# Optimization experiments

Hardware: AMD Instinct MI355X
Metric: run time of the kernel (lower is better)

Reference implementation:

```python
import jax, jax.numpy as jnp
import numpy as np

B, S, Y = 2, 4, 4          # samples, n_views (B*S = BS), voxel height vox_xyz_size[1]
BS = B * S

def _bilinear(feat, coords):
    # feat: [C,H,W]; coords: [N,2] normalized (x,y); OOB handled by the valid mask
    C, H, W = feat.shape
    gx, gy = coords[:, 0], coords[:, 1]
    ix = (gx + 1.0) * 0.5 * (W - 1)
    iy = (gy + 1.0) * 0.5 * (H - 1)
    x0 = jnp.floor(ix); y0 = jnp.floor(iy)
    wx = ix - x0; wy = iy - y0
    x0i = jnp.clip(x0.astype(jnp.int32), 0, W - 1); x1i = jnp.clip(x0i + 1, 0, W - 1)
    y0i = jnp.clip(y0.astype(jnp.int32), 0, H - 1); y1i = jnp.clip(y0i + 1, 0, H - 1)
    v00 = feat[:, y0i, x0i]; v01 = feat[:, y0i, x1i]
    v10 = feat[:, y1i, x0i]; v11 = feat[:, y1i, x1i]
    out = (v00 * (1 - wx) * (1 - wy) + v01 * wx * (1 - wy)
           + v10 * (1 - wx) * wy + v11 * wx * wy)            # [C,N]
    valid = (gx >= -1) & (gx <= 1) & (gy >= -1) & (gy <= 1)   # [N]
    return out, valid

def _scale(feat, coords, Zs, Xs, w, b):
    # feat: [BS,C,H,W]; coords: [BS, Y*Zs*Xs, 2]; w: [Co, C*Y]; b: [Co]
    C = feat.shape[1]
    samp, valid = jax.vmap(_bilinear)(feat, coords)           # [BS,C,N], [BS,N]
    samp = samp.reshape(BS, C, Y, Zs * Xs)
    masked = samp * valid.reshape(BS, 1, Y, Zs * Xs).astype(samp.dtype)
    v = masked.reshape(B, S, C * Y, Zs * Xs).max(axis=1)      # max-pool across views
    v = v.reshape(B, C * Y, Zs, Xs)                           # BEV grid
    bev = jax.nn.silu(jnp.einsum('bizx,oi->bozx', v, w) + b[None, :, None, None])
    return bev, valid

def setup_inputs():
    key = jax.random.key(0)
    ks = jax.random.split(key, 9)
    f = jnp.float32
    x3 = jax.random.normal(ks[0], (BS, 256, 64, 64), f)
    x4 = jax.random.normal(ks[1], (BS, 512, 32, 32), f)
    x5 = jax.random.normal(ks[2], (BS, 1024, 16, 16), f)
    coords_s2 = jax.random.uniform(ks[3], (BS, Y * 64 * 64, 2), f) * 2.4 - 1.2
    coords_s4 = jax.random.uniform(ks[4], (BS, Y * 32 * 32, 2), f) * 2.4 - 1.2
    coords_s8 = jax.random.uniform(ks[5], (BS, Y * 16 * 16, 2), f) * 2.4 - 1.2
    w2 = jax.random.normal(ks[6], (256, 256 * Y), f) * 0.02
    b2 = jnp.zeros((256,), f)
    w4 = jax.random.normal(ks[7], (512, 512 * Y), f) * 0.02
    b4 = jnp.zeros((512,), f)
    w8 = jax.random.normal(ks[8], (1024, 1024 * Y), f) * 0.02
    b8 = jnp.zeros((1024,), f)
    return {"x3": x3, "x4": x4, "x5": x5,
            "coords_s2": coords_s2, "coords_s4": coords_s4, "coords_s8": coords_s8,
            "w2": w2, "b2": b2, "w4": w4, "b4": b4, "w8": w8, "b8": b8}

def reference(x3, x4, x5, coords_s2, coords_s4, coords_s8, w2, b2, w4, b4, w8, b8):
    bev2, valid2 = _scale(x3, coords_s2, 64, 64, w2, b2)
    bev4, _ = _scale(x4, coords_s4, 32, 32, w4, b4)
    bev8, _ = _scale(x5, coords_s8, 16, 16, w8, b8)
    valid_vox_mask = valid2.reshape(B, S, -1).max(axis=1).astype(jnp.float32)
    return bev2, bev4, bev8, valid_vox_mask
```

## Files before the change

kernel.cpp:

```cpp
#include <hip/hip_runtime.h>
#include <hip/hip_bf16.h>
#include <math.h>

namespace {

typedef short short8 __attribute__((ext_vector_type(8)));
typedef float floatx4 __attribute__((ext_vector_type(4)));
typedef unsigned short ushort4v __attribute__((ext_vector_type(4)));
typedef unsigned short ushort8v __attribute__((ext_vector_type(8)));

__device__ __forceinline__ unsigned short f2bf(float x) {
    union { float f; unsigned u; } a; a.f = x;
    unsigned r = a.u + 0x7fff + ((a.u >> 16) & 1);
    return (unsigned short)(r >> 16);
}
__device__ __forceinline__ float bf2f(unsigned short h) {
    union { unsigned u; float f; } a; a.u = ((unsigned)h) << 16;
    return a.f;
}
__device__ __forceinline__ unsigned f2h(float x) {
    _Float16 h = (_Float16)x;
    unsigned short u; __builtin_memcpy(&u, &h, 2);
    return u;
}
__device__ __forceinline__ float h2f(unsigned u) {
    unsigned short us = (unsigned short)u;
    _Float16 h; __builtin_memcpy(&h, &us, 2);
    return (float)h;
}

__device__ __forceinline__ void transp_tile(
    const float* __restrict__ in, unsigned short* __restrict__ out,
    int C, int P, int bs, int pBase, int cBase, int tid, float (*tile)[33])
{
    int tx = tid & 31;
    int ty = tid >> 5;
    const float* ip = in + ((size_t)bs * C + cBase) * P + pBase;
    #pragma unroll
    for (int r = 0; r < 32; r += 8)
        tile[ty + r][tx] = ip[(size_t)(ty + r) * P + tx];
    __syncthreads();
    unsigned short* op = out + ((size_t)bs * P + pBase) * C + cBase;
    #pragma unroll
    for (int r = 0; r < 32; r += 8)
        op[(size_t)(ty + r) * C + tx] = f2bf(tile[tx][ty + r]);
}

__device__ __forceinline__ void coord_prep(
    const float* __restrict__ coords, uint4* __restrict__ table, int Wd, int idx)
{
    float2 g = ((const float2*)coords)[idx];
    uint4 e;
    bool valid = (g.x >= -1.f) && (g.x <= 1.f) && (g.y >= -1.f) && (g.y <= 1.f);
    if (!valid) {
        e.x = 0xFFFFFFFFu; e.y = 0u; e.z = 0u; e.w = 0u;
    } else {
        float ix = (g.x + 1.f) * 0.5f * (float)(Wd - 1);
        float iy = (g.y + 1.f) * 0.5f * (float)(Wd - 1);
        float x0f = floorf(ix), y0f = floorf(iy);
        float wx = ix - x0f, wy = iy - y0f;
        int x0 = min(max((int)x0f, 0), Wd - 1);
        int x1 = min(x0 + 1, Wd - 1);
        int y0 = min(max((int)y0f, 0), Wd - 1);
        int y1 = min(y0 + 1, Wd - 1);
        unsigned p00 = y0 * Wd + x0, p01 = y0 * Wd + x1;
        unsigned p10 = y1 * Wd + x0, p11 = y1 * Wd + x1;
        e.x = p00 | (p01 << 16);
        e.y = p10 | (p11 << 16);
        e.z = f2h((1.f - wx) * (1.f - wy)) | (f2h(wx * (1.f - wy)) << 16);
        e.w = f2h((1.f - wx) * wy)         | (f2h(wx * wy) << 16);
    }
    table[idx] = e;
}

__global__ __launch_bounds__(256) void prep_all(
    const float* __restrict__ x3, const float* __restrict__ x4, const float* __restrict__ x5,
    unsigned short* __restrict__ f2, unsigned short* __restrict__ f4, unsigned short* __restrict__ f8,
    const float* __restrict__ w2, const float* __restrict__ w4, const float* __restrict__ w8,
    unsigned short* __restrict__ o2, unsigned short* __restrict__ o4, unsigned short* __restrict__ o8,
    const float* __restrict__ c2, const float* __restrict__ c4, const float* __restrict__ c8,
    uint4* __restrict__ t2, uint4* __restrict__ t4, uint4* __restrict__ t8,
    float* __restrict__ mask)
{
    __shared__ float tile[32][33];
    int bid = blockIdx.x;
    int tid = threadIdx.x;
    if (bid < 8192) {
        int bs = bid >> 10, r = bid & 1023;
        transp_tile(x3, f2, 256, 4096, bs, (r & 127) * 32, (r >> 7) * 32, tid, tile);
    } else if (bid < 12288) {
        int local = bid - 8192;
        int bs = local >> 9, r = local & 511;
        transp_tile(x4, f4, 512, 1024, bs, (r & 31) * 32, (r >> 5) * 32, tid, tile);
    } else if (bid < 14336) {
        int local = bid - 12288;
        int bs = local >> 8, r = local & 255;
        transp_tile(x5, f8, 1024, 256, bs, (r & 7) * 32, (r >> 3) * 32, tid, tile);
    } else if (bid < 19712) {
        int local = bid - 14336;
        const float* in; unsigned short* out;
        if (local < 256)       { in = w2; out = o2; }
        else if (local < 1280) { in = w4; out = o4; local -= 256; }
        else                   { in = w8; out = o8; local -= 1280; }
        long idx = ((long)local * 256 + tid) * 4;
        float4 v = *reinterpret_cast<const float4*>(in + idx);
        ushort4 u;
        u.x = f2bf(v.x); u.y = f2bf(v.y); u.z = f2bf(v.z); u.w = f2bf(v.w);
        *reinterpret_cast<ushort4*>(out + idx) = u;
    } else if (bid < 20224) {
        coord_prep(c2, t2, 64, (bid - 19712) * 256 + tid);
    } else if (bid < 20352) {
        coord_prep(c4, t4, 32, (bid - 20224) * 256 + tid);
    } else if (bid < 20384) {
        coord_prep(c8, t8, 16, (bid - 20352) * 256 + tid);
    } else {
        int idx = (bid - 20384) * 256 + tid;
        int n = idx & 16383;
        int b = idx >> 14;
        float best = 0.f;
        #pragma unroll
        for (int s = 0; s < 4; ++s) {
            float2 g = ((const float2*)c2)[(size_t)(b * 4 + s) * 16384 + n];
            bool valid = (g.x >= -1.f) && (g.x <= 1.f) && (g.y >= -1.f) && (g.y <= 1.f);
            if (valid) best = 1.f;
        }
        mask[idx] = best;
    }
}

__device__ __forceinline__ void sample_core(
    const unsigned short* __restrict__ featT, const uint4* __restrict__ table,
    unsigned short* __restrict__ vout,
    int P, int M, int C, int logM, int b, int m, int chunk, int lane)
{
    int c = chunk * 256 + lane * 4;
    unsigned short outv[16];
    #pragma unroll
    for (int y = 0; y < 4; ++y) {
        float bst0 = -3.4e38f, bst1 = -3.4e38f, bst2 = -3.4e38f, bst3 = -3.4e38f;
        bool anyinv = false;
        #pragma unroll
        for (int s = 0; s < 4; ++s) {
            int bs = b * 4 + s;
            uint4 e = table[(((size_t)bs * 4 + y) << logM) + m];
            if ((e.x & 0xffffu) == 0xffffu) { anyinv = true; continue; }
            unsigned p00 = e.x & 0xffffu, p01 = e.x >> 16;
            unsigned p10 = e.y & 0xffffu, p11 = e.y >> 16;
            float w00 = h2f(e.z & 0xffffu), w01 = h2f(e.z >> 16);
            float w10 = h2f(e.w & 0xffffu), w11 = h2f(e.w >> 16);
            const unsigned short* fp = featT + (size_t)bs * P * C + c;
            ushort4v u00 = *reinterpret_cast<const ushort4v*>(fp + (size_t)p00 * C);
            ushort4v u01 = *reinterpret_cast<const ushort4v*>(fp + (size_t)p01 * C);
            ushort4v u10 = *reinterpret_cast<const ushort4v*>(fp + (size_t)p10 * C);
            ushort4v u11 = *reinterpret_cast<const ushort4v*>(fp + (size_t)p11 * C);
            bst0 = fmaxf(bst0, bf2f(u00[0]) * w00 + bf2f(u01[0]) * w01 + bf2f(u10[0]) * w10 + bf2f(u11[0]) * w11);
            bst1 = fmaxf(bst1, bf2f(u00[1]) * w00 + bf2f(u01[1]) * w01 + bf2f(u10[1]) * w10 + bf2f(u11[1]) * w11);
            bst2 = fmaxf(bst2, bf2f(u00[2]) * w00 + bf2f(u01[2]) * w01 + bf2f(u10[2]) * w10 + bf2f(u11[2]) * w11);
            bst3 = fmaxf(bst3, bf2f(u00[3]) * w00 + bf2f(u01[3]) * w01 + bf2f(u10[3]) * w10 + bf2f(u11[3]) * w11);
        }
        if (anyinv) {
            bst0 = fmaxf(bst0, 0.f); bst1 = fmaxf(bst1, 0.f);
            bst2 = fmaxf(bst2, 0.f); bst3 = fmaxf(bst3, 0.f);
        }
        outv[0 * 4 + y] = f2bf(bst0);
        outv[1 * 4 + y] = f2bf(bst1);
        outv[2 * 4 + y] = f2bf(bst2);
        outv[3 * 4 + y] = f2bf(bst3);
    }
    size_t base = (((size_t)b << logM) + m) * ((size_t)C * 4) + (size_t)chunk * 1024 + lane * 16;
    ushort8v o0, o1;
    #pragma unroll
    for (int t = 0; t < 8; ++t) { o0[t] = outv[t]; o1[t] = outv[8 + t]; }
    *reinterpret_cast<ushort8v*>(vout + base)     = o0;
    *reinterpret_cast<ushort8v*>(vout + base + 8) = o1;
}

__global__ __launch_bounds__(256) void sample_all(
    const unsigned short* __restrict__ f2, const unsigned short* __restrict__ f4,
    const unsigned short* __restrict__ f8,
    const uint4* __restrict__ t2, const uint4* __restrict__ t4, const uint4* __restrict__ t8,
    unsigned short* __restrict__ v2, unsigned short* __restrict__ v4,
    unsigned short* __restrict__ v8)
{
    int bid = blockIdx.x;
    int w = threadIdx.x >> 6;
    int lane = threadIdx.x & 63;
    if (bid < 2048) {
        sample_core(f2, t2, v2, 4096, 4096, 256, 12,
                    bid & 1, (bid >> 1) * 4 + w, 0, lane);
    } else if (bid < 3072) {
        int local = bid - 2048;
        sample_core(f4, t4, v4, 1024, 1024, 512, 10,
                    local & 1, (local >> 1) * 2 + (w >> 1), w & 1, lane);
    } else {
        int local = bid - 3072;
        sample_core(f8, t8, v8, 256, 256, 1024, 8,
                    local & 1, local >> 1, w, lane);
    }
}

#define GLOAD(s, it) do { \
    w##s##a = *reinterpret_cast<const float4*>(Wp + (size_t)row0 * K + (it) * 64 + kc); \
    w##s##b = *reinterpret_cast<const float4*>(Wp + (size_t)(row0 + 32) * K + (it) * 64 + kc); \
    v##s##a = *reinterpret_cast<const float4*>(Vp + (size_t)row0 * K + (it) * 64 + kc); \
    v##s##b = *reinterpret_cast<const float4*>(Vp + (size_t)(row0 + 32) * K + (it) * 64 + kc); \
} while (0)

#define LSTORE(s, buf) do { \
    *reinterpret_cast<float4*>(&As[buf][row0 * 72 + kc]) = w##s##a; \
    *reinterpret_cast<float4*>(&As[buf][(row0 + 32) * 72 + kc]) = w##s##b; \
    *reinterpret_cast<float4*>(&Bs[buf][row0 * 72 + kc]) = v##s##a; \
    *reinterpret_cast<float4*>(&Bs[buf][(row0 + 32) * 72 + kc]) = v##s##b; \
} while (0)

#define MFMA_STEP(buf) do { \
    _Pragma("unroll") \
    for (int kss = 0; kss < 64; kss += 32) { \
        short8 af0 = *reinterpret_cast<const short8*>(&As[buf][(wo + lr) * 72 + kss + quad * 8]); \
        short8 af1 = *reinterpret_cast<const short8*>(&As[buf][(wo + 16 + lr) * 72 + kss + quad * 8]); \
        short8 bf0 = *reinterpret_cast<const short8*>(&Bs[buf][(wm + lr) * 72 + kss + quad * 8]); \
        short8 bf1 = *reinterpret_cast<const short8*>(&Bs[buf][(wm + 16 + lr) * 72 + kss + quad * 8]); \
        acc[0][0] = __builtin_amdgcn_mfma_f32_16x16x32_bf16(af0, bf0, acc[0][0], 0, 0, 0); \
        acc[0][1] = __builtin_amdgcn_mfma_f32_16x16x32_bf16(af0, bf1, acc[0][1], 0, 0, 0); \
        acc[1][0] = __builtin_amdgcn_mfma_f32_16x16x32_bf16(af1, bf0, acc[1][0], 0, 0, 0); \
        acc[1][1] = __builtin_amdgcn_mfma_f32_16x16x32_bf16(af1, bf1, acc[1][1], 0, 0, 0); \
    } \
} while (0)

__device__ __forceinline__ void gemm_tile(
    const unsigned short* __restrict__ Wb, const unsigned short* __restrict__ Vb,
    const float* __restrict__ bias, float* __restrict__ out, float* __restrict__ partial,
    int N, int K, int M, int kSplit, int local, int logMt, int logNt,
    int tid, unsigned short (*As)[64 * 72], unsigned short (*Bs)[64 * 72])
{
    const int mTile = local & ((1 << logMt) - 1);
    const int rest  = local >> logMt;
    const int oTile = rest & ((1 << logNt) - 1);
    const int z     = rest >> logNt;
    const int b = z & 1;
    const int ks = z >> 1;
    const int Kspan = K / kSplit;
    const int nIter = Kspan >> 6;

    const int mBase = mTile * 64;
    const int oBase = oTile * 64;
    const int lane = tid & 63;
    const int wave = tid >> 6;
    const int wo = (wave >> 1) * 32;
    const int wm = (wave & 1) * 32;
    const int quad = lane >> 4;
    const int lr = lane & 15;
    const int row0 = tid >> 3;
    const int kc = (tid & 7) * 8;

    const unsigned short* Wp = Wb + (size_t)oBase * K + ks * Kspan;
    const unsigned short* Vp = Vb + ((size_t)b * M + mBase) * K + ks * Kspan;

    floatx4 acc[2][2] = {};
    float4 w0a, w0b, v0a, v0b;
    float4 w1a, w1b, v1a, v1b;

    GLOAD(0, 0);
    LSTORE(0, 0);
    GLOAD(1, 1);
    __syncthreads();

    for (int it = 0; it < nIter; it += 2) {
        MFMA_STEP(0);
        LSTORE(1, 1);
        if (it + 2 < nIter) GLOAD(0, it + 2);
        __syncthreads();
        MFMA_STEP(1);
        if (it + 2 < nIter) {
            LSTORE(0, 0);
            if (it + 3 < nIter) GLOAD(1, it + 3);
            __syncthreads();
        }
    }

    if (kSplit == 1) {
        #pragma unroll
        for (int i = 0; i < 2; ++i)
            #pragma unroll
            for (int r = 0; r < 4; ++r) {
                int o = oBase + wo + i * 16 + quad * 4 + r;
                float bi = bias[o];
                #pragma unroll
                for (int j = 0; j < 2; ++j) {
                    int m = mBase + wm + j * 16 + lr;
                    float x = acc[i][j][r] + bi;
                    out[((size_t)b * N + o) * M + m] = x / (1.f + __expf(-x));
                }
            }
    } else {
        float* pp = partial + (size_t)z * N * M;
        #pragma unroll
        for (int i = 0; i < 2; ++i)
            #pragma unroll
            for (int r = 0; r < 4; ++r) {
                int o = oBase + wo + i * 16 + quad * 4 + r;
                #pragma unroll
                for (int j = 0; j < 2; ++j) {
                    int m = mBase + wm + j * 16 + lr;
                    pp[(size_t)o * M + m] = acc[i][j][r];
                }
            }
    }
}

__global__ __launch_bounds__(256) void gemm_all(
    const unsigned short* __restrict__ w2b, const unsigned short* __restrict__ w4b,
    const unsigned short* __restrict__ w8b,
    const unsigned short* __restrict__ v2, const unsigned short* __restrict__ v4,
    const unsigned short* __restrict__ v8,
    const float* __restrict__ b2, float* __restrict__ bev2,
    float* __restrict__ part4, float* __restrict__ part8)
{
    __shared__ __align__(16) unsigned short As[2][64 * 72];
    __shared__ __align__(16) unsigned short Bs[2][64 * 72];
    int bid = blockIdx.x;
    int tid = threadIdx.x;
    if (bid < 512)
        gemm_tile(w2b, v2, b2, bev2, nullptr, 256, 1024, 4096, 1, bid, 6, 2, tid, As, Bs);
    else if (bid < 1536)
        gemm_tile(w4b, v4, nullptr, nullptr, part4, 512, 2048, 1024, 4, bid - 512, 4, 3, tid, As, Bs);
    else
        gemm_tile(w8b, v8, nullptr, nullptr, part8, 1024, 4096, 256, 8, bid - 1536, 2, 4, tid, As, Bs);
}

__device__ __forceinline__ void reduce_seg(
    const float* __restrict__ partial, const float* __restrict__ bias,
    float* __restrict__ out, int N, int M, int kSplit, size_t idx)
{
    int m4 = M >> 2;
    int mi = (int)(idx % m4);
    int o  = (int)((idx / m4) % N);
    int b  = (int)(idx / ((size_t)m4 * N));
    size_t base = ((size_t)b * N + o) * M + (size_t)mi * 4;
    size_t stride = (size_t)2 * N * M;
    float4 s = *reinterpret_cast<const float4*>(partial + base);
    for (int k = 1; k < kSplit; ++k) {
        float4 t = *reinterpret_cast<const float4*>(partial + base + (size_t)k * stride);
        s.x += t.x; s.y += t.y; s.z += t.z; s.w += t.w;
    }
    float bi = bias[o];
    float xs[4] = {s.x + bi, s.y + bi, s.z + bi, s.w + bi};
    float4 r;
    r.x = xs[0] / (1.f + __expf(-xs[0]));
    r.y = xs[1] / (1.f + __expf(-xs[1]));
    r.z = xs[2] / (1.f + __expf(-xs[2]));
    r.w = xs[3] / (1.f + __expf(-xs[3]));
    *reinterpret_cast<float4*>(out + base) = r;
}

__global__ __launch_bounds__(256) void reduce_all(
    const float* __restrict__ part4, const float* __restrict__ b4, float* __restrict__ bev4,
    const float* __restrict__ part8, const float* __restrict__ b8, float* __restrict__ bev8)
{
    int bid = blockIdx.x;
    int tid = threadIdx.x;
    if (bid < 1024)
        reduce_seg(part4, b4, bev4, 512, 1024, 4, (size_t)bid * 256 + tid);
    else
        reduce_seg(part8, b8, bev8, 1024, 256, 8, (size_t)(bid - 1024) * 256 + tid);
}

}

extern "C" void kernel_launch(void* const* d_in, const int* in_sizes, int n_in,
                              void* d_out, int out_size, void* d_ws, size_t ws_size,
                              hipStream_t stream)
{
    const float* x3 = (const float*)d_in[0];
    const float* x4 = (const float*)d_in[1];
    const float* x5 = (const float*)d_in[2];
    const float* c2 = (const float*)d_in[3];
    const float* c4 = (const float*)d_in[4];
    const float* c8 = (const float*)d_in[5];
    const float* w2 = (const float*)d_in[6];
    const float* b2 = (const float*)d_in[7];
    const float* w4 = (const float*)d_in[8];
    const float* b4 = (const float*)d_in[9];
    const float* w8 = (const float*)d_in[10];
    const float* b8 = (const float*)d_in[11];

    float* out  = (float*)d_out;
    float* bev2 = out;
    float* bev4 = bev2 + (long)2 * 256 * 64 * 64;
    float* bev8 = bev4 + (long)2 * 512 * 32 * 32;
    float* mask = bev8 + (long)2 * 1024 * 16 * 16;

    char* ws = (char*)d_ws;
    unsigned short* f2v  = (unsigned short*)(ws);
    unsigned short* f4v  = (unsigned short*)(ws + (16L << 20));
    unsigned short* f8v  = (unsigned short*)(ws + (24L << 20));
    unsigned short* v2v  = (unsigned short*)(ws + (28L << 20));
    unsigned short* v4v  = (unsigned short*)(ws + (44L << 20));
    unsigned short* v8v  = (unsigned short*)(ws + (52L << 20));
    unsigned short* w2bf = (unsigned short*)(ws + (56L << 20));
    unsigned short* w4bf = (unsigned short*)(ws + (57L << 20));
    unsigned short* w8bf = (unsigned short*)(ws + (59L << 20));
    float*          part4 = (float*)(ws + (68L << 20));
    float*          part8 = (float*)(ws + (84L << 20));
    uint4*          t2v   = (uint4*)(ws + (100L << 20));
    uint4*          t4v   = (uint4*)(ws + (102L << 20));
    uint4*          t8v   = (uint4*)(ws + (102L << 20) + (1L << 19));

    prep_all<<<dim3(20512), 256, 0, stream>>>(
        x3, x4, x5, f2v, f4v, f8v,
        w2, w4, w8, w2bf, w4bf, w8bf,
        c2, c4, c8, t2v, t4v, t8v, mask);
    sample_all<<<dim3(3584), 256, 0, stream>>>(
        f2v, f4v, f8v, t2v, t4v, t8v, v2v, v4v, v8v);
    gemm_all<<<dim3(2560), 256, 0, stream>>>(
        w2bf, w4bf, w8bf, v2v, v4v, v8v, b2, bev2, part4, part8);
    reduce_all<<<dim3(1536), 256, 0, stream>>>(
        part4, b4, bev4, part8, b8, bev8);
}
```

Before: 204.2 us.

## Stagger per-scale stages across kernels to overlap prep, sampling and GEMM

Result: slower. 210.0 us (+2.8%).

```diff
diff --git a/kernel.cpp b/kernel.cpp
--- a/kernel.cpp
+++ b/kernel.cpp
@@ -73,59 +73,14 @@
     table[idx] = e;
 }
 
-__global__ __launch_bounds__(256) void prep_all(
-    const float* __restrict__ x3, const float* __restrict__ x4, const float* __restrict__ x5,
-    unsigned short* __restrict__ f2, unsigned short* __restrict__ f4, unsigned short* __restrict__ f8,
-    const float* __restrict__ w2, const float* __restrict__ w4, const float* __restrict__ w8,
-    unsigned short* __restrict__ o2, unsigned short* __restrict__ o4, unsigned short* __restrict__ o8,
-    const float* __restrict__ c2, const float* __restrict__ c4, const float* __restrict__ c8,
-    uint4* __restrict__ t2, uint4* __restrict__ t4, uint4* __restrict__ t8,
-    float* __restrict__ mask)
-{
-    __shared__ float tile[32][33];
-    int bid = blockIdx.x;
-    int tid = threadIdx.x;
-    if (bid < 8192) {
-        int bs = bid >> 10, r = bid & 1023;
-        transp_tile(x3, f2, 256, 4096, bs, (r & 127) * 32, (r >> 7) * 32, tid, tile);
-    } else if (bid < 12288) {
-        int local = bid - 8192;
-        int bs = local >> 9, r = local & 511;
-        transp_tile(x4, f4, 512, 1024, bs, (r & 31) * 32, (r >> 5) * 32, tid, tile);
-    } else if (bid < 14336) {
-        int local = bid - 12288;
-        int bs = local >> 8, r = local & 255;
-        transp_tile(x5, f8, 1024, 256, bs, (r & 7) * 32, (r >> 3) * 32, tid, tile);
-    } else if (bid < 19712) {
-        int local = bid - 14336;
-        const float* in; unsigned short* out;
-        if (local < 256)       { in = w2; out = o2; }
-        else if (local < 1280) { in = w4; out = o4; local -= 256; }
-        else                   { in = w8; out = o8; local -= 1280; }
-        long idx = ((long)local * 256 + tid) * 4;
-        float4 v = *reinterpret_cast<const float4*>(in + idx);
-        ushort4 u;
-        u.x = f2bf(v.x); u.y = f2bf(v.y); u.z = f2bf(v.z); u.w = f2bf(v.w);
-        *reinterpret_cast<ushort4*>(out + idx) = u;
-    } else if (bid < 20224) {
-        coord_prep(c2, t2, 64, (bid - 19712) * 256 + tid);
-    } else if (bid < 20352) {
-        coord_prep(c4, t4, 32, (bid - 20224) * 256 + tid);
-    } else if (bid < 20384) {
-        coord_prep(c8, t8, 16, (bid - 20352) * 256 + tid);
-    } else {
-        int idx = (bid - 20384) * 256 + tid;
-        int n = idx & 16383;
-        int b = idx >> 14;
-        float best = 0.f;
-        #pragma unroll
-        for (int s = 0; s < 4; ++s) {
-            float2 g = ((const float2*)c2)[(size_t)(b * 4 + s) * 16384 + n];
-            bool valid = (g.x >= -1.f) && (g.x <= 1.f) && (g.y >= -1.f) && (g.y <= 1.f);
-            if (valid) best = 1.f;
-        }
-        mask[idx] = best;
-    }
+__device__ __forceinline__ void cvt_seg(
+    const float* __restrict__ in, unsigned short* __restrict__ out, int local, int tid)
+{
+    long idx = ((long)local * 256 + tid) * 4;
+    float4 v = *reinterpret_cast<const float4*>(in + idx);
+    ushort4 u;
+    u.x = f2bf(v.x); u.y = f2bf(v.y); u.z = f2bf(v.z); u.w = f2bf(v.w);
+    *reinterpret_cast<ushort4*>(out + idx) = u;
 }
 
 __device__ __forceinline__ void sample_core(
@@ -175,30 +130,6 @@
     *reinterpret_cast<ushort8v*>(vout + base + 8) = o1;
 }
 
-__global__ __launch_bounds__(256) void sample_all(
-    const unsigned short* __restrict__ f2, const unsigned short* __restrict__ f4,
-    const unsigned short* __restrict__ f8,
-    const uint4* __restrict__ t2, const uint4* __restrict__ t4, const uint4* __restrict__ t8,
-    unsigned short* __restrict__ v2, unsigned short* __restrict__ v4,
-    unsigned short* __restrict__ v8)
-{
-    int bid = blockIdx.x;
-    int w = threadIdx.x >> 6;
-    int lane = threadIdx.x & 63;
-    if (bid < 2048) {
-        sample_core(f2, t2, v2, 4096, 4096, 256, 12,
-                    bid & 1, (bid >> 1) * 4 + w, 0, lane);
-    } else if (bid < 3072) {
-        int local = bid - 2048;
-        sample_core(f4, t4, v4, 1024, 1024, 512, 10,
-                    local & 1, (local >> 1) * 2 + (w >> 1), w & 1, lane);
-    } else {
-        int local = bid - 3072;
-        sample_core(f8, t8, v8, 256, 256, 1024, 8,
-                    local & 1, local >> 1, w, lane);
-    }
-}
-
 #define GLOAD(s, it) do { \
     w##s##a = *reinterpret_cast<const float4*>(Wp + (size_t)row0 * K + (it) * 64 + kc); \
     w##s##b = *reinterpret_cast<const float4*>(Wp + (size_t)(row0 + 32) * K + (it) * 64 + kc); \
@@ -308,24 +239,113 @@
     }
 }
 
-__global__ __launch_bounds__(256) void gemm_all(
-    const unsigned short* __restrict__ w2b, const unsigned short* __restrict__ w4b,
-    const unsigned short* __restrict__ w8b,
-    const unsigned short* __restrict__ v2, const unsigned short* __restrict__ v4,
-    const unsigned short* __restrict__ v8,
-    const float* __restrict__ b2, float* __restrict__ bev2,
-    float* __restrict__ part4, float* __restrict__ part8)
+__global__ __launch_bounds__(256) void prep_s2(
+    const float* __restrict__ x3, unsigned short* __restrict__ f2,
+    const float* __restrict__ w2, unsigned short* __restrict__ o2,
+    const float* __restrict__ c2, uint4* __restrict__ t2,
+    float* __restrict__ mask)
+{
+    __shared__ float tile[32][33];
+    int bid = blockIdx.x;
+    int tid = threadIdx.x;
+    if (bid < 8192) {
+        int bs = bid >> 10, r = bid & 1023;
+        transp_tile(x3, f2, 256, 4096, bs, (r & 127) * 32, (r >> 7) * 32, tid, tile);
+    } else if (bid < 8448) {
+        cvt_seg(w2, o2, bid - 8192, tid);
+    } else if (bid < 8960) {
+        coord_prep(c2, t2, 64, (bid - 8448) * 256 + tid);
+    } else {
+        int idx = (bid - 8960) * 256 + tid;
+        int n = idx & 16383;
+        int b = idx >> 14;
+        float best = 0.f;
+        #pragma unroll
+        for (int s = 0; s < 4; ++s) {
+            float2 g = ((const float2*)c2)[(size_t)(b * 4 + s) * 16384 + n];
+            bool valid = (g.x >= -1.f) && (g.x <= 1.f) && (g.y >= -1.f) && (g.y <= 1.f);
+            if (valid) best = 1.f;
+        }
+        mask[idx] = best;
+    }
+}
+
+__global__ __launch_bounds__(256) void samp2_prep48(
+    const unsigned short* __restrict__ f2, const uint4* __restrict__ t2,
+    unsigned short* __restrict__ v2,
+    const float* __restrict__ x4, const float* __restrict__ x5,
+    unsigned short* __restrict__ f4, unsigned short* __restrict__ f8,
+    const float* __restrict__ w4, const float* __restrict__ w8,
+    unsigned short* __restrict__ o4, unsigned short* __restrict__ o8,
+    const float* __restrict__ c4, const float* __restrict__ c8,
+    uint4* __restrict__ t4, uint4* __restrict__ t8)
+{
+    __shared__ float tile[32][33];
+    int bid = blockIdx.x;
+    int tid = threadIdx.x;
+    int w = tid >> 6;
+    int lane = tid & 63;
+    if (bid < 2048) {
+        sample_core(f2, t2, v2, 4096, 4096, 256, 12,
+                    bid & 1, (bid >> 1) * 4 + w, 0, lane);
+    } else if (bid < 6144) {
+        int local = bid - 2048;
+        int bs = local >> 9, r = local & 511;
+        transp_tile(x4, f4, 512, 1024, bs, (r & 31) * 32, (r >> 5) * 32, tid, tile);
+    } else if (bid < 8192) {
+        int local = bid - 6144;
+        int bs = local >> 8, r = local & 255;
+        transp_tile(x5, f8, 1024, 256, bs, (r & 7) * 32, (r >> 3) * 32, tid, tile);
+    } else if (bid < 9216) {
+        cvt_seg(w4, o4, bid - 8192, tid);
+    } else if (bid < 13312) {
+        cvt_seg(w8, o8, bid - 9216, tid);
+    } else if (bid < 13440) {
+        coord_prep(c4, t4, 32, (bid - 13312) * 256 + tid);
+    } else {
+        coord_prep(c8, t8, 16, (bid - 13440) * 256 + tid);
+    }
+}
+
+__global__ __launch_bounds__(256) void samp48_gemm2(
+    const unsigned short* __restrict__ f4, const unsigned short* __restrict__ f8,
+    const uint4* __restrict__ t4, const uint4* __restrict__ t8,
+    unsigned short* __restrict__ v4, unsigned short* __restrict__ v8,
+    const unsigned short* __restrict__ w2b, const unsigned short* __restrict__ v2,
+    const float* __restrict__ b2, float* __restrict__ bev2)
 {
     __shared__ __align__(16) unsigned short As[2][64 * 72];
     __shared__ __align__(16) unsigned short Bs[2][64 * 72];
     int bid = blockIdx.x;
     int tid = threadIdx.x;
-    if (bid < 512)
-        gemm_tile(w2b, v2, b2, bev2, nullptr, 256, 1024, 4096, 1, bid, 6, 2, tid, As, Bs);
-    else if (bid < 1536)
-        gemm_tile(w4b, v4, nullptr, nullptr, part4, 512, 2048, 1024, 4, bid - 512, 4, 3, tid, As, Bs);
+    int w = tid >> 6;
+    int lane = tid & 63;
+    if (bid < 1024) {
+        sample_core(f4, t4, v4, 1024, 1024, 512, 10,
+                    bid & 1, (bid >> 1) * 2 + (w >> 1), w & 1, lane);
+    } else if (bid < 1536) {
+        int local = bid - 1024;
+        sample_core(f8, t8, v8, 256, 256, 1024, 8,
+                    local & 1, local >> 1, w, lane);
+    } else {
+        gemm_tile(w2b, v2, b2, bev2, nullptr, 256, 1024, 4096, 1,
+                  bid - 1536, 6, 2, tid, As, Bs);
+    }
+}
+
+__global__ __launch_bounds__(256) void gemm48(
+    const unsigned short* __restrict__ w4b, const unsigned short* __restrict__ w8b,
+    const unsigned short* __restrict__ v4, const unsigned short* __restrict__ v8,
+    float* __restrict__ part4, float* __restrict__ part8)
+{
+    __shared__ __align__(16) unsigned short As[2][64 * 72];
+    __shared__ __align__(16) unsigned short Bs[2][64 * 72];
+    int bid = blockIdx.x;
+    int tid = threadIdx.x;
+    if (bid < 1024)
+        gemm_tile(w4b, v4, nullptr, nullptr, part4, 512, 2048, 1024, 4, bid, 4, 3, tid, As, Bs);
     else
-        gemm_tile(w8b, v8, nullptr, nullptr, part8, 1024, 4096, 256, 8, bid - 1536, 2, 4, tid, As, Bs);
+        gemm_tile(w8b, v8, nullptr, nullptr, part8, 1024, 4096, 256, 8, bid - 1024, 2, 4, tid, As, Bs);
 }
 
 __device__ __forceinline__ void reduce_seg(
@@ -406,14 +426,11 @@
     uint4*          t4v   = (uint4*)(ws + (102L << 20));
     uint4*          t8v   = (uint4*)(ws + (102L << 20) + (1L << 19));
 
-    prep_all<<<dim3(20512), 256, 0, stream>>>(
-        x3, x4, x5, f2v, f4v, f8v,
-        w2, w4, w8, w2bf, w4bf, w8bf,
-        c2, c4, c8, t2v, t4v, t8v, mask);
-    sample_all<<<dim3(3584), 256, 0, stream>>>(
-        f2v, f4v, f8v, t2v, t4v, t8v, v2v, v4v, v8v);
-    gemm_all<<<dim3(2560), 256, 0, stream>>>(
-        w2bf, w4bf, w8bf, v2v, v4v, v8v, b2, bev2, part4, part8);
-    reduce_all<<<dim3(1536), 256, 0, stream>>>(
-        part4, b4, bev4, part8, b8, bev8);
-}
+    prep_s2<<<dim3(9088), 256, 0, stream>>>(x3, f2v, w2, w2bf, c2, t2v, mask);
+    samp2_prep48<<<dim3(13472), 256, 0, stream>>>(
+        f2v, t2v, v2v, x4, x5, f4v, f8v, w4, w8, w4bf, w8bf, c4, c8, t4v, t8v);
+    samp48_gemm2<<<dim3(2048), 256, 0, stream>>>(
+        f4v, f8v, t4v, t8v, v4v, v8v, w2bf, v2v, b2, bev2);
+    gemm48<<<dim3(2048), 256, 0, stream>>>(w4bf, w8bf, v4v, v8v, part4, part8);
+    reduce_all<<<dim3(1536), 256, 0, stream>>>(part4, b4, bev4, part8, b8, bev8);
+}
```

## Enlarge GEMM tiles to 128x128 with single LDS buffer and reduced split-K

Applied to the files above, without the earlier changes.

Result: faster. 197.4 us (-3.4%).

```diff
diff --git a/kernel.cpp b/kernel.cpp
--- a/kernel.cpp
+++ b/kernel.cpp
@@ -73,6 +73,16 @@
     table[idx] = e;
 }
 
+__device__ __forceinline__ void cvt_seg(
+    const float* __restrict__ in, unsigned short* __restrict__ out, int local, int tid)
+{
+    long idx = ((long)local * 256 + tid) * 4;
+    float4 v = *reinterpret_cast<const float4*>(in + idx);
+    ushort4 u;
+    u.x = f2bf(v.x); u.y = f2bf(v.y); u.z = f2bf(v.z); u.w = f2bf(v.w);
+    *reinterpret_cast<ushort4*>(out + idx) = u;
+}
+
 __global__ __launch_bounds__(256) void prep_all(
     const float* __restrict__ x3, const float* __restrict__ x4, const float* __restrict__ x5,
     unsigned short* __restrict__ f2, unsigned short* __restrict__ f4, unsigned short* __restrict__ f8,
@@ -102,11 +112,7 @@
         if (local < 256)       { in = w2; out = o2; }
         else if (local < 1280) { in = w4; out = o4; local -= 256; }
         else                   { in = w8; out = o8; local -= 1280; }
-        long idx = ((long)local * 256 + tid) * 4;
-        float4 v = *reinterpret_cast<const float4*>(in + idx);
-        ushort4 u;
-        u.x = f2bf(v.x); u.y = f2bf(v.y); u.z = f2bf(v.z); u.w = f2bf(v.w);
-        *reinterpret_cast<ushort4*>(out + idx) = u;
+        cvt_seg(in, out, local, tid);
     } else if (bid < 20224) {
         coord_prep(c2, t2, 64, (bid - 19712) * 256 + tid);
     } else if (bid < 20352) {
@@ -199,39 +205,11 @@
     }
 }
 
-#define GLOAD(s, it) do { \
-    w##s##a = *reinterpret_cast<const float4*>(Wp + (size_t)row0 * K + (it) * 64 + kc); \
-    w##s##b = *reinterpret_cast<const float4*>(Wp + (size_t)(row0 + 32) * K + (it) * 64 + kc); \
-    v##s##a = *reinterpret_cast<const float4*>(Vp + (size_t)row0 * K + (it) * 64 + kc); \
-    v##s##b = *reinterpret_cast<const float4*>(Vp + (size_t)(row0 + 32) * K + (it) * 64 + kc); \
-} while (0)
-
-#define LSTORE(s, buf) do { \
-    *reinterpret_cast<float4*>(&As[buf][row0 * 72 + kc]) = w##s##a; \
-    *reinterpret_cast<float4*>(&As[buf][(row0 + 32) * 72 + kc]) = w##s##b; \
-    *reinterpret_cast<float4*>(&Bs[buf][row0 * 72 + kc]) = v##s##a; \
-    *reinterpret_cast<float4*>(&Bs[buf][(row0 + 32) * 72 + kc]) = v##s##b; \
-} while (0)
-
-#define MFMA_STEP(buf) do { \
-    _Pragma("unroll") \
-    for (int kss = 0; kss < 64; kss += 32) { \
-        short8 af0 = *reinterpret_cast<const short8*>(&As[buf][(wo + lr) * 72 + kss + quad * 8]); \
-        short8 af1 = *reinterpret_cast<const short8*>(&As[buf][(wo + 16 + lr) * 72 + kss + quad * 8]); \
-        short8 bf0 = *reinterpret_cast<const short8*>(&Bs[buf][(wm + lr) * 72 + kss + quad * 8]); \
-        short8 bf1 = *reinterpret_cast<const short8*>(&Bs[buf][(wm + 16 + lr) * 72 + kss + quad * 8]); \
-        acc[0][0] = __builtin_amdgcn_mfma_f32_16x16x32_bf16(af0, bf0, acc[0][0], 0, 0, 0); \
-        acc[0][1] = __builtin_amdgcn_mfma_f32_16x16x32_bf16(af0, bf1, acc[0][1], 0, 0, 0); \
-        acc[1][0] = __builtin_amdgcn_mfma_f32_16x16x32_bf16(af1, bf0, acc[1][0], 0, 0, 0); \
-        acc[1][1] = __builtin_amdgcn_mfma_f32_16x16x32_bf16(af1, bf1, acc[1][1], 0, 0, 0); \
-    } \
-} while (0)
-
-__device__ __forceinline__ void gemm_tile(
+__device__ __forceinline__ void gemm_tile128(
     const unsigned short* __restrict__ Wb, const unsigned short* __restrict__ Vb,
     const float* __restrict__ bias, float* __restrict__ out, float* __restrict__ partial,
     int N, int K, int M, int kSplit, int local, int logMt, int logNt,
-    int tid, unsigned short (*As)[64 * 72], unsigned short (*Bs)[64 * 72])
+    int tid, unsigned short* As, unsigned short* Bs)
 {
     const int mTile = local & ((1 << logMt) - 1);
     const int rest  = local >> logMt;
@@ -242,12 +220,12 @@
     const int Kspan = K / kSplit;
     const int nIter = Kspan >> 6;
 
-    const int mBase = mTile * 64;
-    const int oBase = oTile * 64;
+    const int mBase = mTile * 128;
+    const int oBase = oTile * 128;
     const int lane = tid & 63;
     const int wave = tid >> 6;
-    const int wo = (wave >> 1) * 32;
-    const int wm = (wave & 1) * 32;
+    const int wo = (wave >> 1) * 64;
+    const int wm = (wave & 1) * 64;
     const int quad = lane >> 4;
     const int lr = lane & 15;
     const int row0 = tid >> 3;
@@ -256,37 +234,65 @@
     const unsigned short* Wp = Wb + (size_t)oBase * K + ks * Kspan;
     const unsigned short* Vp = Vb + ((size_t)b * M + mBase) * K + ks * Kspan;
 
-    floatx4 acc[2][2] = {};
-    float4 w0a, w0b, v0a, v0b;
-    float4 w1a, w1b, v1a, v1b;
-
-    GLOAD(0, 0);
-    LSTORE(0, 0);
-    GLOAD(1, 1);
-    __syncthreads();
-
-    for (int it = 0; it < nIter; it += 2) {
-        MFMA_STEP(0);
-        LSTORE(1, 1);
-        if (it + 2 < nIter) GLOAD(0, it + 2);
+    floatx4 acc[4][4] = {};
+    float4 wr0, wr1, wr2, wr3, vr0, vr1, vr2, vr3;
+
+#define GLOAD128(it) do { \
+    wr0 = *reinterpret_cast<const float4*>(Wp + (size_t)(row0      ) * K + (it) * 64 + kc); \
+    wr1 = *reinterpret_cast<const float4*>(Wp + (size_t)(row0 + 32 ) * K + (it) * 64 + kc); \
+    wr2 = *reinterpret_cast<const float4*>(Wp + (size_t)(row0 + 64 ) * K + (it) * 64 + kc); \
+    wr3 = *reinterpret_cast<const float4*>(Wp + (size_t)(row0 + 96 ) * K + (it) * 64 + kc); \
+    vr0 = *reinterpret_cast<const float4*>(Vp + (size_t)(row0      ) * K + (it) * 64 + kc); \
+    vr1 = *reinterpret_cast<const float4*>(Vp + (size_t)(row0 + 32 ) * K + (it) * 64 + kc); \
+    vr2 = *reinterpret_cast<const float4*>(Vp + (size_t)(row0 + 64 ) * K + (it) * 64 + kc); \
+    vr3 = *reinterpret_cast<const float4*>(Vp + (size_t)(row0 + 96 ) * K + (it) * 64 + kc); \
+} while (0)
+
+#define LSTORE128() do { \
+    *reinterpret_cast<float4*>(&As[(row0      ) * 72 + kc]) = wr0; \
+    *reinterpret_cast<float4*>(&As[(row0 + 32 ) * 72 + kc]) = wr1; \
+    *reinterpret_cast<float4*>(&As[(row0 + 64 ) * 72 + kc]) = wr2; \
+    *reinterpret_cast<float4*>(&As[(row0 + 96 ) * 72 + kc]) = wr3; \
+    *reinterpret_cast<float4*>(&Bs[(row0      ) * 72 + kc]) = vr0; \
+    *reinterpret_cast<float4*>(&Bs[(row0 + 32 ) * 72 + kc]) = vr1; \
+    *reinterpret_cast<float4*>(&Bs[(row0 + 64 ) * 72 + kc]) = vr2; \
+    *reinterpret_cast<float4*>(&Bs[(row0 + 96 ) * 72 + kc]) = vr3; \
+} while (0)
+
+    GLOAD128(0);
+    LSTORE128();
+
+    for (int it = 0; it < nIter; ++it) {
         __syncthreads();
-        MFMA_STEP(1);
-        if (it + 2 < nIter) {
-            LSTORE(0, 0);
-            if (it + 3 < nIter) GLOAD(1, it + 3);
-            __syncthreads();
+        if (it + 1 < nIter) GLOAD128(it + 1);
+        #pragma unroll
+        for (int kss = 0; kss < 64; kss += 32) {
+            short8 af[4], bf[4];
+            #pragma unroll
+            for (int i = 0; i < 4; ++i)
+                af[i] = *reinterpret_cast<const short8*>(&As[(wo + i * 16 + lr) * 72 + kss + quad * 8]);
+            #pragma unroll
+            for (int j = 0; j < 4; ++j)
+                bf[j] = *reinterpret_cast<const short8*>(&Bs[(wm + j * 16 + lr) * 72 + kss + quad * 8]);
+            #pragma unroll
+            for (int i = 0; i < 4; ++i)
+                #pragma unroll
+                for (int j = 0; j < 4; ++j)
+                    acc[i][j] = __builtin_amdgcn_mfma_f32_16x16x32_bf16(af[i], bf[j], acc[i][j], 0, 0, 0);
         }
+        __syncthreads();
+        if (it + 1 < nIter) LSTORE128();
     }
 
     if (kSplit == 1) {
         #pragma unroll
-        for (int i = 0; i < 2; ++i)
+        for (int i = 0; i < 4; ++i)
             #pragma unroll
             for (int r = 0; r < 4; ++r) {
                 int o = oBase + wo + i * 16 + quad * 4 + r;
                 float bi = bias[o];
                 #pragma unroll
-                for (int j = 0; j < 2; ++j) {
+                for (int j = 0; j < 4; ++j) {
                     int m = mBase + wm + j * 16 + lr;
                     float x = acc[i][j][r] + bi;
                     out[((size_t)b * N + o) * M + m] = x / (1.f + __expf(-x));
@@ -295,20 +301,22 @@
     } else {
         float* pp = partial + (size_t)z * N * M;
         #pragma unroll
-        for (int i = 0; i < 2; ++i)
+        for (int i = 0; i < 4; ++i)
             #pragma unroll
             for (int r = 0; r < 4; ++r) {
                 int o = oBase + wo + i * 16 + quad * 4 + r;
                 #pragma unroll
-                for (int j = 0; j < 2; ++j) {
+                for (int j = 0; j < 4; ++j) {
                     int m = mBase + wm + j * 16 + lr;
                     pp[(size_t)o * M + m] = acc[i][j][r];
                 }
             }
     }
-}
-
-__global__ __launch_bounds__(256) void gemm_all(
+#undef GLOAD128
+#undef LSTORE128
+}
+
+__global__ __launch_bounds__(256, 2) void gemm_all(
     const unsigned short* __restrict__ w2b, const unsigned short* __restrict__ w4b,
     const unsigned short* __restrict__ w8b,
     const unsigned short* __restrict__ v2, const unsigned short* __restrict__ v4,
@@ -316,16 +324,16 @@
     const float* __restrict__ b2, float* __restrict__ bev2,
     float* __restrict__ part4, float* __restrict__ part8)
 {
-    __shared__ __align__(16) unsigned short As[2][64 * 72];
-    __shared__ __align__(16) unsigned short Bs[2][64 * 72];
+    __shared__ __align__(16) unsigned short As[128 * 72];
+    __shared__ __align__(16) unsigned short Bs[128 * 72];
     int bid = blockIdx.x;
     int tid = threadIdx.x;
-    if (bid < 512)
-        gemm_tile(w2b, v2, b2, bev2, nullptr, 256, 1024, 4096, 1, bid, 6, 2, tid, As, Bs);
-    else if (bid < 1536)
-        gemm_tile(w4b, v4, nullptr, nullptr, part4, 512, 2048, 1024, 4, bid - 512, 4, 3, tid, As, Bs);
+    if (bid < 128)
+        gemm_tile128(w2b, v2, b2, bev2, nullptr, 256, 1024, 4096, 1, bid, 5, 1, tid, As, Bs);
+    else if (bid < 256)
+        gemm_tile128(w4b, v4, nullptr, nullptr, part4, 512, 2048, 1024, 2, bid - 128, 3, 2, tid, As, Bs);
     else
-        gemm_tile(w8b, v8, nullptr, nullptr, part8, 1024, 4096, 256, 8, bid - 1536, 2, 4, tid, As, Bs);
+        gemm_tile128(w8b, v8, nullptr, nullptr, part8, 1024, 4096, 256, 4, bid - 256, 1, 3, tid, As, Bs);
 }
 
 __device__ __forceinline__ void reduce_seg(
@@ -360,9 +368,9 @@
     int bid = blockIdx.x;
     int tid = threadIdx.x;
     if (bid < 1024)
-        reduce_seg(part4, b4, bev4, 512, 1024, 4, (size_t)bid * 256 + tid);
+        reduce_seg(part4, b4, bev4, 512, 1024, 2, (size_t)bid * 256 + tid);
     else
-        reduce_seg(part8, b8, bev8, 1024, 256, 8, (size_t)(bid - 1024) * 256 + tid);
+        reduce_seg(part8, b8, bev8, 1024, 256, 4, (size_t)(bid - 1024) * 256 + tid);
 }
 
 }
@@ -412,7 +420,7 @@
         c2, c4, c8, t2v, t4v, t8v, mask);
     sample_all<<<dim3(3584), 256, 0, stream>>>(
         f2v, f4v, f8v, t2v, t4v, t8v, v2v, v4v, v8v);
-    gemm_all<<<dim3(2560), 256, 0, stream>>>(
+    gemm_all<<<dim3(384), 256, 0, stream>>>(
         w2bf, w4bf, w8bf, v2v, v4v, v8v, b2, bev2, part4, part8);
     reduce_all<<<dim3(1536), 256, 0, stream>>>(
         part4, b4, bev4, part8, b8, bev8);
```
